# Kernel tuning notes

Hardware: AMD Instinct MI355X
Metric: run time of the kernel (lower is better)

## Reference

```python
import jax, jax.numpy as jnp
import numpy as np

B, T, V = 8, 2048, 4096
BEAM = 8      # beam_size
BLANK = 0     # blank_id=0 in CTCBeamDecoder
TMP = 1.0     # temperature self.tmp


def setup_inputs() -> dict:
    key = jax.random.key(0)
    k1, k2 = jax.random.split(key)
    logits = jax.random.normal(k1, (B, T, V), dtype=jnp.float32)
    # valid frame counts in [T//2, T]
    lengths = jax.random.randint(k2, (B,), T // 2, T + 1).astype(jnp.int32)
    return {"logits": logits, "lengths": lengths}


def _beam_search_single(logP, length):
    """CTC beam search over alignments (no LM) for one utterance.
    logP: [T, V] log-probs, length: scalar valid frame count.
    Returns (collapsed_tokens [T] padded with -1, out_len, best_score).
    """
    scores0, toks0 = jax.lax.top_k(logP[0], BEAM)              # [BEAM]
    toks0 = toks0.astype(jnp.int32)
    bp0 = jnp.zeros((BEAM,), jnp.int32)

    def step(scores, xs):
        t, logp_t = xs
        cand = scores[:, None] + logp_t[None, :]               # [BEAM, V]
        new_scores, flat_idx = jax.lax.top_k(cand.reshape(-1), BEAM)
        bp = (flat_idx // V).astype(jnp.int32)
        tok = (flat_idx % V).astype(jnp.int32)
        valid = t < length
        new_scores = jnp.where(valid, new_scores, scores)
        bp = jnp.where(valid, bp, jnp.arange(BEAM, dtype=jnp.int32))
        tok = jnp.where(valid, tok, jnp.full((BEAM,), BLANK, jnp.int32))
        return new_scores, (tok, bp)

    ts = jnp.arange(1, T)
    final_scores, (toks, bps) = jax.lax.scan(step, scores0, (ts, logP[1:]))
    toks = jnp.concatenate([toks0[None], toks], axis=0)        # [T, BEAM]
    bps = jnp.concatenate([bp0[None], bps], axis=0)            # [T, BEAM]

    # backtrace best beam (index 0 after final top_k)
    def back(beam, xs):
        tok_t, bp_t = xs
        return bp_t[beam], tok_t[beam]
    _, path = jax.lax.scan(back, jnp.int32(0), (toks, bps), reverse=True)  # [T] in time order

    # CTC collapse: drop blanks and consecutive repeats, restrict to valid frames
    tpos = jnp.arange(T)
    prev = jnp.concatenate([jnp.array([-1], jnp.int32), path[:-1]])
    keep = (path != BLANK) & (path != prev) & (tpos < length)
    out_len = keep.sum().astype(jnp.int32)
    pos = jnp.cumsum(keep) - 1                                  # target slot for kept tokens
    idx = jnp.where(keep, pos, T)                               # dump non-kept into slot T
    out = jnp.full((T + 1,), -1, jnp.int32).at[idx].set(jnp.where(keep, path, -1))
    return out[:T], out_len, final_scores[0]


def reference(logits, lengths):
    # logits/tmp then log_softmax (the tensorized part of the torch module)
    logP = jax.nn.log_softmax(logits / TMP, axis=-1)            # [B, T, V]
    tokens, out_lens, best_scores = jax.vmap(_beam_search_single)(logP, lengths)
    return tokens, out_lens, best_scores, logP
```

## Files before the change

### kernel.cpp

```cpp
#include <hip/hip_runtime.h>
#include <cmath>

#define NB 8
#define NT 2048
#define NV 4096
#define NK 12

__device__ __forceinline__ void lds_fence() {
  asm volatile("s_waitcnt lgkmcnt(0)" ::: "memory");
}

__global__ __launch_bounds__(64) void lsm_top12_kernel(
    const float* __restrict__ logits,
    float* __restrict__ out_logP,
    float* __restrict__ topPf,
    int* __restrict__ topI)
{
  const int row  = blockIdx.x;
  const int lane = threadIdx.x;
  const float4* __restrict__ x4 = (const float4*)(logits + (size_t)row * NV);

  float m = -INFINITY;
  #pragma unroll 4
  for (int k = 0; k < 16; ++k) {
    float4 f = x4[lane + (k << 6)];
    m = fmaxf(m, fmaxf(fmaxf(f.x, f.y), fmaxf(f.z, f.w)));
  }
  #pragma unroll
  for (int off = 32; off > 0; off >>= 1) m = fmaxf(m, __shfl_xor(m, off, 64));

  float a0 = 0.0f, a1 = 0.0f, a2 = 0.0f, a3 = 0.0f;
  #pragma unroll 4
  for (int k = 0; k < 16; ++k) {
    float4 f = x4[lane + (k << 6)];
    a0 += __expf(f.x - m);
    a1 += __expf(f.y - m);
    a2 += __expf(f.z - m);
    a3 += __expf(f.w - m);
  }
  float accf = (a0 + a1) + (a2 + a3);
  #pragma unroll
  for (int off = 32; off > 0; off >>= 1) accf += __shfl_xor(accf, off, 64);
  const float L32 = logf(accf);

  float lv[NK]; int li[NK];
  #pragma unroll
  for (int z = 0; z < NK; ++z) { lv[z] = -INFINITY; li[z] = 0x7FFFFFFF; }

#define INS(VAL, IDX)                                                       \
  do {                                                                      \
    float _v = (VAL); int _i = (IDX);                                       \
    if (_v > lv[NK - 1]) {                                                  \
      lv[NK - 1] = _v; li[NK - 1] = _i;                                     \
      for (int z = NK - 1; z > 0; --z)                                      \
        if (lv[z] > lv[z - 1]) {                                            \
          float tv = lv[z]; lv[z] = lv[z - 1]; lv[z - 1] = tv;              \
          int   ti = li[z]; li[z] = li[z - 1]; li[z - 1] = ti;              \
        }                                                                   \
    }                                                                       \
  } while (0)

  float4* __restrict__ orow4 = (float4*)(out_logP + (size_t)row * NV);
  #pragma unroll 2
  for (int k = 0; k < 16; ++k) {
    float4 f = x4[lane + (k << 6)];
    int vb = (lane + (k << 6)) << 2;
    float4 o;
    o.x = (f.x - m) - L32;
    o.y = (f.y - m) - L32;
    o.z = (f.z - m) - L32;
    o.w = (f.w - m) - L32;
    orow4[lane + (k << 6)] = o;
    INS(o.x, vb); INS(o.y, vb + 1); INS(o.z, vb + 2); INS(o.w, vb + 3);
  }
#undef INS

  float mv = 0.0f; int mi = 0;
  #pragma unroll
  for (int r = 0; r < NK; ++r) {
    float cv = lv[0]; int ci = li[0];
    #pragma unroll
    for (int off = 32; off > 0; off >>= 1) {
      float ov = __shfl_xor(cv, off, 64);
      int   oi = __shfl_xor(ci, off, 64);
      if (ov > cv || (ov == cv && oi < ci)) { cv = ov; ci = oi; }
    }
    if (r == 0)    { mv = cv; mi = ci; }
    if (lane == r) { mv = cv; mi = ci; }
    if (lv[0] == cv && li[0] == ci) {
      for (int z = 0; z < NK - 1; ++z) { lv[z] = lv[z + 1]; li[z] = li[z + 1]; }
      lv[NK - 1] = -INFINITY; li[NK - 1] = 0x7FFFFFFF;
    }
  }
  if (lane < NK) {
    topPf[(size_t)row * NK + lane] = mv;
    topI [(size_t)row * NK + lane] = mi;
  }
}


#define LOADROW(P, V, R)                                                      \
  do {                                                                        \
    const int _r = (R) < NT ? (R) : (NT - 1);                                 \
    P = Pb[(size_t)_r * NK + j_l];                                            \
    V = Ib[(size_t)_r * NK + j_l];                                            \
  } while (0)

#define STEP(T, PV, VV)                                                       \
  do {                                                                        \
    const float cand = s + (PV);              \
    unsigned int cb = __float_as_uint(cand);                                  \
    cb ^= (unsigned int)((int)cb >> 31) | 0x80000000u;                        \
    const unsigned int flat = (unsigned int)((i_l << 12) | (VV));             \
    const unsigned long long key =                                            \
        ((unsigned long long)cb << 15) | (unsigned long long)(0x7FFFu ^ flat);\
    const unsigned int klo = (unsigned int)key;                               \
    const unsigned int khi = (unsigned int)(key >> 32);                       \
    int rank = 0;                                                             \
    _Pragma("unroll")                                                         \
    for (int mm = 0; mm < 31; ++mm) {                                         \
      const unsigned int olo =                                                \
          (unsigned int)__builtin_amdgcn_readlane((int)klo, mm);              \
      const unsigned int ohi =                                                \
          (unsigned int)__builtin_amdgcn_readlane((int)khi, mm);              \
      const unsigned long long ok = ((unsigned long long)ohi << 32) | olo;    \
      rank += (ok > key) ? 1 : 0;                                             \
    }                                                                         \
      \
    const bool win = active && (rank < 8);                                    \
    const int sloti = win ? ((T) * 8 + rank) : (NT * 8 + lane);               \
    tokbp[sloti] = (unsigned short)(((VV) << 3) | i_l);                       \
    const int dst4 = win ? (rank << 2) : park4;                               \
    const int pushed =                                                        \
        __builtin_amdgcn_ds_permute(dst4, __float_as_int(cand));              \
    const float w0 = __uint_as_float((unsigned)__builtin_amdgcn_readlane(pushed, 0)); \
    const float w1 = __uint_as_float((unsigned)__builtin_amdgcn_readlane(pushed, 1)); \
    const float w2 = __uint_as_float((unsigned)__builtin_amdgcn_readlane(pushed, 2)); \
    const float w3 = __uint_as_float((unsigned)__builtin_amdgcn_readlane(pushed, 3)); \
    const float w4 = __uint_as_float((unsigned)__builtin_amdgcn_readlane(pushed, 4)); \
    const float w5 = __uint_as_float((unsigned)__builtin_amdgcn_readlane(pushed, 5)); \
    const float w6 = __uint_as_float((unsigned)__builtin_amdgcn_readlane(pushed, 6)); \
    const float w7 = __uint_as_float((unsigned)__builtin_amdgcn_readlane(pushed, 7)); \
    const float sA_ = b0 ? w1 : w0;                                           \
    const float sB_ = b0 ? w3 : w2;                                           \
    const float sC_ = b0 ? w5 : w4;                                           \
    const float sD_ = b0 ? w7 : w6;                                           \
    const float sE_ = b1 ? sB_ : sA_;                                         \
    const float sF_ = b1 ? sD_ : sC_;                                         \
    s = b2 ? sF_ : sE_;                                                       \
  } while (0)

__global__ __launch_bounds__(64) void beam_kernel(
    const float* __restrict__ topPf,
    const int* __restrict__ topI,
    const int* __restrict__ lengths,
    float* __restrict__ out_tok,
    float* __restrict__ out_lenA,
    float* __restrict__ out_scr)
{
  const int b    = blockIdx.x;
  const int lane = threadIdx.x;

  __shared__ unsigned short tokbp[NT * 8 + 64];
  __shared__ unsigned short pathA[NT];

  int len = lengths[b];
  if (len < 1) len = 1;
  if (len > NT) len = NT;

  int i_l = 0, j_l = 0; bool active = false;
  {
    int c = 0;
    #pragma unroll
    for (int i = 0; i < 8; ++i) {
      const int cnt = 12 / (i + 1);
      if (lane >= c && lane < c + cnt) { i_l = i; j_l = lane - c; active = true; }
      c += cnt;
    }
  }
  const bool b0 = (i_l & 1) != 0;
  const bool b1 = (i_l & 2) != 0;
  const bool b2 = (i_l & 4) != 0;
  const int  park4 = (32 + (lane & 31)) << 2;

  const float* __restrict__ Pb = topPf + (size_t)b * NT * NK;
  const int*   __restrict__ Ib = topI  + (size_t)b * NT * NK;

  float s = Pb[i_l];
  if (lane < 8) tokbp[lane] = (unsigned short)(Ib[lane] << 3);

  float pA0, pA1, pA2, pA3, pB0, pB1, pB2, pB3;
  int   vA0, vA1, vA2, vA3, vB0, vB1, vB2, vB3;
  LOADROW(pA0, vA0, 1); LOADROW(pA1, vA1, 2);
  LOADROW(pA2, vA2, 3); LOADROW(pA3, vA3, 4);
  LOADROW(pB0, vB0, 5); LOADROW(pB1, vB1, 6);
  LOADROW(pB2, vB2, 7); LOADROW(pB3, vB3, 8);

  int t = 1;
  for (; t + 7 < len; t += 8) {
    STEP(t,     pA0, vA0);
    STEP(t + 1, pA1, vA1);
    STEP(t + 2, pA2, vA2);
    STEP(t + 3, pA3, vA3);
    LOADROW(pA0, vA0, t + 8);  LOADROW(pA1, vA1, t + 9);
    LOADROW(pA2, vA2, t + 10); LOADROW(pA3, vA3, t + 11);
    STEP(t + 4, pB0, vB0);
    STEP(t + 5, pB1, vB1);
    STEP(t + 6, pB2, vB2);
    STEP(t + 7, pB3, vB3);
    LOADROW(pB0, vB0, t + 12); LOADROW(pB1, vB1, t + 13);
    LOADROW(pB2, vB2, t + 14); LOADROW(pB3, vB3, t + 15);
  }
  if (t     < len) STEP(t,     pA0, vA0);
  if (t + 1 < len) STEP(t + 1, pA1, vA1);
  if (t + 2 < len) STEP(t + 2, pA2, vA2);
  if (t + 3 < len) STEP(t + 3, pA3, vA3);
  if (t + 4 < len) STEP(t + 4, pB0, vB0);
  if (t + 5 < len) STEP(t + 5, pB1, vB1);
  if (t + 6 < len) STEP(t + 6, pB2, vB2);

  lds_fence();
  if (lane == 0) {
    const uint4* __restrict__ rows = (const uint4*)tokbp;
#define EXT(R)                                                                \
    do {                                                                      \
      const unsigned long long half = (beam < 4)                              \
          ? (((unsigned long long)(R).y << 32) | (R).x)                       \
          : (((unsigned long long)(R).w << 32) | (R).z);                      \
      const int e = (int)((half >> ((beam & 3) << 4)) & 0xFFFFu);             \
      pathA[bt] = (unsigned short)(e >> 3);                                   \
      beam = e & 7;                                                           \
      --bt;                                                                   \
    } while (0)
    int beam = 0;
    int bt = len - 1;
    uint4 r0 = rows[bt];
    uint4 r1 = rows[bt >= 1 ? bt - 1 : 0];
    uint4 r2 = rows[bt >= 2 ? bt - 2 : 0];
    uint4 r3 = rows[bt >= 3 ? bt - 3 : 0];
    while (bt >= 7) {
      const uint4 n0 = rows[bt - 4], n1 = rows[bt - 5];
      const uint4 n2 = rows[bt - 6], n3 = rows[bt - 7];
      EXT(r0); EXT(r1); EXT(r2); EXT(r3);
      r0 = n0; r1 = n1; r2 = n2; r3 = n3;
    }
    while (bt >= 0) { const uint4 rr = rows[bt]; EXT(rr); }
#undef EXT
  }
  lds_fence();

  const int CH = NT / 64;
  const int base = lane * CH;
  int cnt = 0;
  for (int k = 0; k < CH; ++k) {
    int tt = base + k;
    if (tt < len) {
      int pt = pathA[tt];
      int pv = (tt > 0) ? (int)pathA[tt - 1] : -1;
      cnt += ((pt != 0) && (pt != pv)) ? 1 : 0;
    }
  }
  int incl = cnt;
  #pragma unroll
  for (int off = 1; off < 64; off <<= 1) {
    int n = __shfl_up(incl, off, 64);
    if (lane >= off) incl += n;
  }
  const int excl  = incl - cnt;
  const int total = __shfl(incl, 63, 64);

  float* __restrict__ ob = out_tok + (size_t)b * NT;
  int pos = excl;
  for (int k = 0; k < CH; ++k) {
    int tt = base + k;
    if (tt < len) {
      int pt = pathA[tt];
      int pv = (tt > 0) ? (int)pathA[tt - 1] : -1;
      if ((pt != 0) && (pt != pv)) { ob[pos] = (float)pt; ++pos; }
    }
  }
  for (int q = total + lane; q < NT; q += 64) ob[q] = -1.0f;

  if (lane == 0) {
    out_lenA[b] = (float)total;
    out_scr[b]  = s;
  }
}

#undef STEP
#undef LOADROW

extern "C" void kernel_launch(void* const* d_in, const int* in_sizes, int n_in,
                              void* d_out, int out_size, void* d_ws, size_t ws_size,
                              hipStream_t stream) {
  (void)in_sizes; (void)n_in; (void)out_size; (void)ws_size;
  const float* logits  = (const float*)d_in[0];
  const int*   lengths = (const int*)d_in[1];

  float* out_tok  = (float*)d_out;
  float* out_lenp = out_tok + NB * NT;
  float* out_scr  = out_lenp + NB;
  float* out_logP = out_scr + NB;

  float* topPf = (float*)d_ws;
  int*   topI  = (int*)(topPf + (size_t)NB * NT * NK);

  lsm_top12_kernel<<<NB * NT, 64, 0, stream>>>(logits, out_logP, topPf, topI);
  beam_kernel<<<NB, 64, 0, stream>>>(topPf, topI, lengths, out_tok, out_lenp, out_scr);
}
```

Before: 1.374 ms.

## Cache logits row in registers and stage beam top-k chunks in LDS

The log-softmax kernel now loads each row's 16 float4 values into registers once, where it previously re-read global memory in three separate passes. The beam kernel stops prefetching per-step candidate rows from global memory into registers. Instead it cooperatively copies 128-step chunks of the top-12 probabilities and indices into shared memory and reads the next step from LDS, with a one-step software prefetch. This targets global-load latency in the serial beam loop. The costs are higher register pressure in the first kernel and a chunk-copy stall every 128 steps.

```diff
diff --git a/kernel.cpp b/kernel.cpp
--- a/kernel.cpp
+++ b/kernel.cpp
@@ -5,6 +5,7 @@
 #define NT 2048
 #define NV 4096
 #define NK 12
+#define CHUNK 128
 
 __device__ __forceinline__ void lds_fence() {
   asm volatile("s_waitcnt lgkmcnt(0)" ::: "memory");
@@ -20,23 +21,24 @@
   const int lane = threadIdx.x;
   const float4* __restrict__ x4 = (const float4*)(logits + (size_t)row * NV);
 
+  float4 r[16];
+  #pragma unroll
+  for (int k = 0; k < 16; ++k) r[k] = x4[lane + (k << 6)];
+
   float m = -INFINITY;
-  #pragma unroll 4
+  #pragma unroll
+  for (int k = 0; k < 16; ++k)
+    m = fmaxf(m, fmaxf(fmaxf(r[k].x, r[k].y), fmaxf(r[k].z, r[k].w)));
+  #pragma unroll
+  for (int off = 32; off > 0; off >>= 1) m = fmaxf(m, __shfl_xor(m, off, 64));
+
+  float a0 = 0.0f, a1 = 0.0f, a2 = 0.0f, a3 = 0.0f;
+  #pragma unroll
   for (int k = 0; k < 16; ++k) {
-    float4 f = x4[lane + (k << 6)];
-    m = fmaxf(m, fmaxf(fmaxf(f.x, f.y), fmaxf(f.z, f.w)));
-  }
-  #pragma unroll
-  for (int off = 32; off > 0; off >>= 1) m = fmaxf(m, __shfl_xor(m, off, 64));
-
-  float a0 = 0.0f, a1 = 0.0f, a2 = 0.0f, a3 = 0.0f;
-  #pragma unroll 4
-  for (int k = 0; k < 16; ++k) {
-    float4 f = x4[lane + (k << 6)];
-    a0 += __expf(f.x - m);
-    a1 += __expf(f.y - m);
-    a2 += __expf(f.z - m);
-    a3 += __expf(f.w - m);
+    a0 += __expf(r[k].x - m);
+    a1 += __expf(r[k].y - m);
+    a2 += __expf(r[k].z - m);
+    a3 += __expf(r[k].w - m);
   }
   float accf = (a0 + a1) + (a2 + a3);
   #pragma unroll
@@ -61,15 +63,14 @@
   } while (0)
 
   float4* __restrict__ orow4 = (float4*)(out_logP + (size_t)row * NV);
-  #pragma unroll 2
+  #pragma unroll
   for (int k = 0; k < 16; ++k) {
-    float4 f = x4[lane + (k << 6)];
-    int vb = (lane + (k << 6)) << 2;
+    const int vb = (lane + (k << 6)) << 2;
     float4 o;
-    o.x = (f.x - m) - L32;
-    o.y = (f.y - m) - L32;
-    o.z = (f.z - m) - L32;
-    o.w = (f.w - m) - L32;
+    o.x = (r[k].x - m) - L32;
+    o.y = (r[k].y - m) - L32;
+    o.z = (r[k].z - m) - L32;
+    o.w = (r[k].w - m) - L32;
     orow4[lane + (k << 6)] = o;
     INS(o.x, vb); INS(o.y, vb + 1); INS(o.z, vb + 2); INS(o.w, vb + 3);
   }
@@ -77,7 +78,7 @@
 
   float mv = 0.0f; int mi = 0;
   #pragma unroll
-  for (int r = 0; r < NK; ++r) {
+  for (int rr = 0; rr < NK; ++rr) {
     float cv = lv[0]; int ci = li[0];
     #pragma unroll
     for (int off = 32; off > 0; off >>= 1) {
@@ -85,8 +86,8 @@
       int   oi = __shfl_xor(ci, off, 64);
       if (ov > cv || (ov == cv && oi < ci)) { cv = ov; ci = oi; }
     }
-    if (r == 0)    { mv = cv; mi = ci; }
-    if (lane == r) { mv = cv; mi = ci; }
+    if (rr == 0)    { mv = cv; mi = ci; }
+    if (lane == rr) { mv = cv; mi = ci; }
     if (lv[0] == cv && li[0] == ci) {
       for (int z = 0; z < NK - 1; ++z) { lv[z] = lv[z + 1]; li[z] = li[z + 1]; }
       lv[NK - 1] = -INFINITY; li[NK - 1] = 0x7FFFFFFF;
@@ -98,13 +99,6 @@
   }
 }
 
-
-#define LOADROW(P, V, R)                                                      \
-  do {                                                                        \
-    const int _r = (R) < NT ? (R) : (NT - 1);                                 \
-    P = Pb[(size_t)_r * NK + j_l];                                            \
-    V = Ib[(size_t)_r * NK + j_l];                                            \
-  } while (0)
 
 #define STEP(T, PV, VV)                                                       \
   do {                                                                        \
@@ -126,7 +120,6 @@
       const unsigned long long ok = ((unsigned long long)ohi << 32) | olo;    \
       rank += (ok > key) ? 1 : 0;                                             \
     }                                                                         \
-      \
     const bool win = active && (rank < 8);                                    \
     const int sloti = win ? ((T) * 8 + rank) : (NT * 8 + lane);               \
     tokbp[sloti] = (unsigned short)(((VV) << 3) | i_l);                       \
@@ -163,6 +156,8 @@
 
   __shared__ unsigned short tokbp[NT * 8 + 64];
   __shared__ unsigned short pathA[NT];
+  __shared__ float pbuf[CHUNK][NK];
+  __shared__ int   ibuf[CHUNK][NK];
 
   int len = lengths[b];
   if (len < 1) len = 1;
@@ -189,35 +184,30 @@
   float s = Pb[i_l];
   if (lane < 8) tokbp[lane] = (unsigned short)(Ib[lane] << 3);
 
-  float pA0, pA1, pA2, pA3, pB0, pB1, pB2, pB3;
-  int   vA0, vA1, vA2, vA3, vB0, vB1, vB2, vB3;
-  LOADROW(pA0, vA0, 1); LOADROW(pA1, vA1, 2);
-  LOADROW(pA2, vA2, 3); LOADROW(pA3, vA3, 4);
-  LOADROW(pB0, vB0, 5); LOADROW(pB1, vB1, 6);
-  LOADROW(pB2, vB2, 7); LOADROW(pB3, vB3, 8);
-
   int t = 1;
-  for (; t + 7 < len; t += 8) {
-    STEP(t,     pA0, vA0);
-    STEP(t + 1, pA1, vA1);
-    STEP(t + 2, pA2, vA2);
-    STEP(t + 3, pA3, vA3);
-    LOADROW(pA0, vA0, t + 8);  LOADROW(pA1, vA1, t + 9);
-    LOADROW(pA2, vA2, t + 10); LOADROW(pA3, vA3, t + 11);
-    STEP(t + 4, pB0, vB0);
-    STEP(t + 5, pB1, vB1);
-    STEP(t + 6, pB2, vB2);
-    STEP(t + 7, pB3, vB3);
-    LOADROW(pB0, vB0, t + 12); LOADROW(pB1, vB1, t + 13);
-    LOADROW(pB2, vB2, t + 14); LOADROW(pB3, vB3, t + 15);
-  }
-  if (t     < len) STEP(t,     pA0, vA0);
-  if (t + 1 < len) STEP(t + 1, pA1, vA1);
-  if (t + 2 < len) STEP(t + 2, pA2, vA2);
-  if (t + 3 < len) STEP(t + 3, pA3, vA3);
-  if (t + 4 < len) STEP(t + 4, pB0, vB0);
-  if (t + 5 < len) STEP(t + 5, pB1, vB1);
-  if (t + 6 < len) STEP(t + 6, pB2, vB2);
+  while (t < len) {
+    const int t0   = t;
+    const int tend = (t0 + CHUNK < len) ? (t0 + CHUNK) : len;
+    const int n4   = (tend - t0) * 3;
+
+    {
+      const float4* __restrict__ gp = (const float4*)(Pb + (size_t)t0 * NK);
+      const int4*   __restrict__ gi = (const int4*)(Ib + (size_t)t0 * NK);
+      float4* __restrict__ lp = (float4*)&pbuf[0][0];
+      int4*   __restrict__ lq = (int4*)&ibuf[0][0];
+      for (int q = lane; q < n4; q += 64) { lp[q] = gp[q]; lq[q] = gi[q]; }
+    }
+
+    float pc = pbuf[0][j_l];
+    int   vc = ibuf[0][j_l];
+    for (; t < tend; ++t) {
+      const int ni = (t + 1 < tend) ? (t + 1 - t0) : (t - t0);
+      const float pn = pbuf[ni][j_l];
+      const int   vn = ibuf[ni][j_l];
+      STEP(t, pc, vc);
+      pc = pn; vc = vn;
+    }
+  }
 
   lds_fence();
   if (lane == 0) {
@@ -288,7 +278,6 @@
 }
 
 #undef STEP
-#undef LOADROW
 
 extern "C" void kernel_launch(void* const* d_in, const int* in_sizes, int n_in,
                               void* d_out, int out_size, void* d_ws, size_t ws_size,
```

Measured after the change: 1.701 ms. +23.8%, slower.
